# Kernel optimization log

Measured on AMD Instinct MI355X. Metric: run time of the kernel, lower is better.

## Reference

```python
import jax, jax.numpy as jnp
import numpy as np

HIDDEN = 4096
N_HEADS = 32
HEAD_DIM = HIDDEN // N_HEADS
MAX_POS = 2048
ROPE_BASE = 10000.0


def _rope_tables(head_dim, max_pos):
    inv_freq = 1.0 / (ROPE_BASE ** (np.arange(0, head_dim, 2, dtype=np.float32) / head_dim))
    t = np.arange(max_pos, dtype=np.float32)
    freqs = np.einsum('i,j->ij', t, inv_freq)          # [max_pos, head_dim//2]
    emb = np.concatenate([freqs, freqs], axis=-1)       # [max_pos, head_dim]
    return jnp.asarray(np.cos(emb)), jnp.asarray(np.sin(emb))


def _rotate_half(x):
    x1, x2 = jnp.split(x, 2, axis=-1)
    return jnp.concatenate([-x2, x1], axis=-1)


def setup_inputs() -> dict:
    key = jax.random.key(0)
    ks = jax.random.split(key, 5)
    B, S = 1, 2048
    hidden_states = jax.random.normal(ks[0], (B, S, HIDDEN), dtype=jnp.float32)
    # additive causal mask (0 on/below diagonal, large negative above)
    causal = jnp.triu(jnp.full((S, S), -1e9, dtype=jnp.float32), k=1)
    attention_mask = causal[None, None, :, :]
    scale = 0.02
    wq = jax.random.normal(ks[1], (HIDDEN, HIDDEN), dtype=jnp.float32) * scale
    wk = jax.random.normal(ks[2], (HIDDEN, HIDDEN), dtype=jnp.float32) * scale
    wv = jax.random.normal(ks[3], (HIDDEN, HIDDEN), dtype=jnp.float32) * scale
    wo = jax.random.normal(ks[4], (HIDDEN, HIDDEN), dtype=jnp.float32) * scale
    position_ids = jnp.arange(S, dtype=jnp.int64 if jax.config.jax_enable_x64 else jnp.int32)[None, :]
    return {"hidden_states": hidden_states, "attention_mask": attention_mask,
            "wq": wq, "wk": wk, "wv": wv, "wo": wo, "position_ids": position_ids}


def reference(hidden_states, attention_mask, wq, wk, wv, wo, position_ids):
    B, S, H = hidden_states.shape
    cos_tab, sin_tab = _rope_tables(HEAD_DIM, MAX_POS)

    def shape_heads(x):  # [B,S,H] -> [B,nH,S,hd]
        return x.reshape(B, S, N_HEADS, HEAD_DIM).transpose(0, 2, 1, 3)

    # QKV projections (torch Linear: x @ W.T, no bias)
    q = shape_heads(hidden_states @ wq.T)
    k = shape_heads(hidden_states @ wk.T)
    v = shape_heads(hidden_states @ wv.T)

    # RoPE
    cos = cos_tab[position_ids][:, None, :, :]  # [B,1,S,hd]
    sin = sin_tab[position_ids][:, None, :, :]
    q = q * cos + _rotate_half(q) * sin
    k = k * cos + _rotate_half(k) * sin

    # scaled dot-product attention
    scale = 1.0 / jnp.sqrt(jnp.float32(HEAD_DIM))
    scores = jnp.einsum('bhqd,bhkd->bhqk', q, k) * scale
    scores = scores + attention_mask  # broadcast over heads
    scores = jnp.maximum(scores, jnp.finfo(scores.dtype).min)
    probs = jax.nn.softmax(scores, axis=-1)
    attn = jnp.einsum('bhqk,bhkd->bhqd', probs, v)

    # merge heads, output projection
    attn = attn.transpose(0, 2, 1, 3).reshape(B, S, H)
    return attn @ wo.T
```

## Files before the change

kernel.cpp:

```cpp
#include <hip/hip_runtime.h>

typedef __bf16 bf16x8 __attribute__((ext_vector_type(8)));
typedef float f32x4 __attribute__((ext_vector_type(4)));

__device__ __forceinline__ ushort f2bf(float f) {
  uint u = __builtin_bit_cast(uint, f);
  u = (u + 0x7fffu + ((u >> 16) & 1u)) >> 16;
  return (ushort)u;
}
__device__ __forceinline__ float bf2f(ushort h) {
  uint u = ((uint)h) << 16;
  return __builtin_bit_cast(float, u);
}

__device__ __forceinline__ void gload16(const ushort* g, ushort* l) {
  __builtin_amdgcn_global_load_lds(
      (const __attribute__((address_space(1))) unsigned int*)(const void*)g,
      (__attribute__((address_space(3))) unsigned int*)(void*)l, 16, 0, 0);
}

__global__ void cvt_f32_bf16_k(const float* __restrict__ in, ushort* __restrict__ out, int n4) {
  int i = blockIdx.x * blockDim.x + threadIdx.x;
  if (i >= n4) return;
  float4 v = reinterpret_cast<const float4*>(in)[i];
  ushort4 o;
  o.x = f2bf(v.x); o.y = f2bf(v.y); o.z = f2bf(v.z); o.w = f2bf(v.w);
  reinterpret_cast<ushort4*>(out)[i] = o;
}

__global__ void rope_tables_k(float* __restrict__ cosT, float* __restrict__ sinT) {
  int i = blockIdx.x * 256 + threadIdx.x;
  int p = i >> 6, j = i & 63;
  float inv = powf(10000.0f, -(float)j / 64.0f);
  float ang = (float)p * inv;
  cosT[i] = cosf(ang);
  sinT[i] = sinf(ang);
}

__global__ void rope_k(ushort* __restrict__ Q, ushort* __restrict__ K,
                       const float* __restrict__ cosT, const float* __restrict__ sinT,
                       const int* __restrict__ pos) {
  int idx = blockIdx.x * 256 + threadIdx.x;
  int s = idx >> 11;
  int rest = idx & 2047;
  int h = rest >> 6, d = rest & 63;
  int p = pos[s];
  float c = cosT[p * 64 + d], sn = sinT[p * 64 + d];
  size_t base = (size_t)s * 4096 + h * 128 + d;
  float q1 = bf2f(Q[base]), q2 = bf2f(Q[base + 64]);
  Q[base]      = f2bf(q1 * c - q2 * sn);
  Q[base + 64] = f2bf(q2 * c + q1 * sn);
  float k1 = bf2f(K[base]), k2 = bf2f(K[base + 64]);
  K[base]      = f2bf(k1 * c - k2 * sn);
  K[base + 64] = f2bf(k2 * c + k1 * sn);
}

template<typename TA, typename TW, int OMODE>
__global__ __launch_bounds__(256) void gemm_bt(const TA* __restrict__ A, const TW* __restrict__ W,
                                               void* __restrict__ Cout) {
  constexpr int K = 4096, N = 4096;
  constexpr bool BF = (sizeof(TA) == 2);
  __shared__ ushort As[128 * 64];
  __shared__ ushort Ws[128 * 64];
  const int tid = threadIdx.x;
  const int w = tid >> 6, lane = tid & 63, g = lane >> 4, r = lane & 15;
  const int wr = w >> 1, wc = w & 1;
  const int id = blockIdx.x;
  const int xcd = id & 7, slot = id >> 3;
  const int nb = (xcd & 3) * 8 + (slot & 7);
  const int mb = (xcd >> 2) * 8 + (slot >> 3);
  const int m0 = mb * 128, n0 = nb * 128;

  f32x4 acc[4][4];
#pragma unroll
  for (int i = 0; i < 4; i++)
#pragma unroll
    for (int j = 0; j < 4; j++) acc[i][j] = f32x4{0.f, 0.f, 0.f, 0.f};

  for (int k0 = 0; k0 < K; k0 += 64) {
    if (k0) __syncthreads();
    if constexpr (BF) {
#pragma unroll
      for (int i = 0; i < 4; i++) {
        int r0 = (w * 4 + i) * 8;
        int row = r0 + (lane >> 3), c = lane & 7;
        int cs = (c ^ (row & 7)) * 8;
        gload16((const ushort*)A + (size_t)(m0 + row) * K + k0 + cs, &As[r0 * 64]);
        gload16((const ushort*)W + (size_t)(n0 + row) * K + k0 + cs, &Ws[r0 * 64]);
      }
    } else {
#pragma unroll
      for (int i = 0; i < 4; i++) {
        int li = tid + i * 256, row = li >> 3, c = li & 7;
        int cs = (c ^ (row & 7)) * 8;
        float4 v0 = *reinterpret_cast<const float4*>(A + (size_t)(m0 + row) * K + k0 + cs);
        float4 v1 = *reinterpret_cast<const float4*>(A + (size_t)(m0 + row) * K + k0 + cs + 4);
        ushort o[8] = {f2bf(v0.x), f2bf(v0.y), f2bf(v0.z), f2bf(v0.w),
                       f2bf(v1.x), f2bf(v1.y), f2bf(v1.z), f2bf(v1.w)};
        *reinterpret_cast<uint4*>(&As[row * 64 + c * 8]) = *reinterpret_cast<uint4*>(o);
      }
#pragma unroll
      for (int i = 0; i < 4; i++) {
        int li = tid + i * 256, row = li >> 3, c = li & 7;
        int cs = (c ^ (row & 7)) * 8;
        float4 v0 = *reinterpret_cast<const float4*>(W + (size_t)(n0 + row) * K + k0 + cs);
        float4 v1 = *reinterpret_cast<const float4*>(W + (size_t)(n0 + row) * K + k0 + cs + 4);
        ushort o[8] = {f2bf(v0.x), f2bf(v0.y), f2bf(v0.z), f2bf(v0.w),
                       f2bf(v1.x), f2bf(v1.y), f2bf(v1.z), f2bf(v1.w)};
        *reinterpret_cast<uint4*>(&Ws[row * 64 + c * 8]) = *reinterpret_cast<uint4*>(o);
      }
    }
    __syncthreads();

#pragma unroll
    for (int kk = 0; kk < 2; kk++) {
      bf16x8 af[4], bfr[4];
#pragma unroll
      for (int mi = 0; mi < 4; mi++) {
        int row = wr * 64 + mi * 16 + r;
        af[mi] = *reinterpret_cast<const bf16x8*>((const char*)As + row * 128 + (((g + kk * 4) ^ (r & 7)) * 16));
      }
#pragma unroll
      for (int nj = 0; nj < 4; nj++) {
        int row = wc * 64 + nj * 16 + r;
        bfr[nj] = *reinterpret_cast<const bf16x8*>((const char*)Ws + row * 128 + (((g + kk * 4) ^ (r & 7)) * 16));
      }
#pragma unroll
      for (int mi = 0; mi < 4; mi++)
#pragma unroll
        for (int nj = 0; nj < 4; nj++)
          acc[mi][nj] = __builtin_amdgcn_mfma_f32_16x16x32_bf16(af[mi], bfr[nj], acc[mi][nj], 0, 0, 0);
    }
  }

  if constexpr (OMODE == 0) {
    float* C = (float*)Cout;
#pragma unroll
    for (int mi = 0; mi < 4; mi++)
#pragma unroll
      for (int nj = 0; nj < 4; nj++)
#pragma unroll
        for (int j = 0; j < 4; j++) {
          int row = m0 + wr * 64 + mi * 16 + g * 4 + j;
          int col = n0 + wc * 64 + nj * 16 + r;
          C[(size_t)row * N + col] = acc[mi][nj][j];
        }
  } else if constexpr (OMODE == 1) {
    ushort* C = (ushort*)Cout;
#pragma unroll
    for (int mi = 0; mi < 4; mi++)
#pragma unroll
      for (int nj = 0; nj < 4; nj++)
#pragma unroll
        for (int j = 0; j < 4; j++) {
          int row = m0 + wr * 64 + mi * 16 + g * 4 + j;
          int col = n0 + wc * 64 + nj * 16 + r;
          C[(size_t)row * N + col] = f2bf(acc[mi][nj][j]);
        }
  } else {
    ushort* C = (ushort*)Cout;
#pragma unroll
    for (int mi = 0; mi < 4; mi++)
#pragma unroll
      for (int nj = 0; nj < 4; nj++) {
        int col = n0 + wc * 64 + nj * 16 + r;
        int row0 = m0 + wr * 64 + mi * 16 + g * 4;
        ushort4 v;
        v.x = f2bf(acc[mi][nj][0]); v.y = f2bf(acc[mi][nj][1]);
        v.z = f2bf(acc[mi][nj][2]); v.w = f2bf(acc[mi][nj][3]);
        *reinterpret_cast<ushort4*>(C + (size_t)col * 2048 + row0) = v;
      }
  }
}

__global__ __launch_bounds__(256) void attn_fwd(const ushort* __restrict__ Q, const ushort* __restrict__ K,
                                                const ushort* __restrict__ Vt, ushort* __restrict__ O) {
  constexpr int S = 2048, HD = 4096;
  __shared__ ushort Ks[2][64 * 128];
  __shared__ ushort Vs[2][128 * 64];
  __shared__ ushort Ps[4][16 * 64];
  const int id = blockIdx.x;
  const int xcd = id & 7, slot = id >> 3;
  const int h = xcd * 4 + (slot & 3);
  const int qx = slot >> 2;
  const int tid = threadIdx.x;
  const int w = tid >> 6, lane = tid & 63, g = lane >> 4, r = lane & 15;
  const float scale = 0.08838834764831845f;
  const int kRow = lane >> 4, kC = lane & 15;
  const int vRow = lane >> 3, vC = lane & 7;

#pragma unroll 1
  for (int pass = 0; pass < 2; ++pass) {
    const int qtile = pass ? (31 - qx) : qx;
    const int qbase = qtile * 64;
    const int nt = qtile + 1;

    bf16x8 qf[4];
    {
      const int qrow = qbase + w * 16 + r;
#pragma unroll
      for (int dc = 0; dc < 4; dc++)
        qf[dc] = *reinterpret_cast<const bf16x8*>(Q + (size_t)qrow * HD + h * 128 + dc * 32 + g * 8);
    }

    f32x4 o[8];
#pragma unroll
    for (int i = 0; i < 8; i++) o[i] = f32x4{0.f, 0.f, 0.f, 0.f};
    float m[4] = {-3e38f, -3e38f, -3e38f, -3e38f};
    float l[4] = {0.f, 0.f, 0.f, 0.f};

    __syncthreads();
#pragma unroll
    for (int i = 0; i < 4; i++) {
      int kr0 = (w * 4 + i) * 4, krow = kr0 + kRow;
      gload16(K + (size_t)krow * HD + h * 128 + (kC ^ (krow & 7)) * 8, &Ks[0][kr0 * 128]);
      int vr0 = (w * 4 + i) * 8, vrow = vr0 + vRow;
      gload16(Vt + (size_t)(h * 128 + vrow) * S + (vC ^ (vrow & 7)) * 8, &Vs[0][vr0 * 64]);
    }

#pragma unroll 1
    for (int t = 0; t < nt; ++t) {
      const int kv0 = t * 64;
      const int buf = t & 1;
      __syncthreads();
      if (t + 1 < nt) {
        const int kvn = kv0 + 64;
#pragma unroll
        for (int i = 0; i < 4; i++) {
          int kr0 = (w * 4 + i) * 4, krow = kr0 + kRow;
          gload16(K + (size_t)(kvn + krow) * HD + h * 128 + (kC ^ (krow & 7)) * 8, &Ks[buf ^ 1][kr0 * 128]);
          int vr0 = (w * 4 + i) * 8, vrow = vr0 + vRow;
          gload16(Vt + (size_t)(h * 128 + vrow) * S + kvn + (vC ^ (vrow & 7)) * 8, &Vs[buf ^ 1][vr0 * 64]);
        }
      }

      f32x4 sc[4];
      __builtin_amdgcn_s_setprio(1);
#pragma unroll
      for (int c = 0; c < 4; c++) {
        f32x4 tacc = f32x4{0.f, 0.f, 0.f, 0.f};
        const int krow = c * 16 + r;
        const char* kb = (const char*)&Ks[buf][0] + krow * 256;
#pragma unroll
        for (int dc = 0; dc < 4; dc++) {
          bf16x8 kf = *reinterpret_cast<const bf16x8*>(kb + ((dc * 64 + g * 16) ^ ((krow & 7) << 4)));
          tacc = __builtin_amdgcn_mfma_f32_16x16x32_bf16(qf[dc], kf, tacc, 0, 0, 0);
        }
        sc[c] = tacc;
      }
      __builtin_amdgcn_s_setprio(0);

#pragma unroll
      for (int c = 0; c < 4; c++) {
        int kvg = kv0 + c * 16 + r;
#pragma unroll
        for (int j = 0; j < 4; j++) {
          int qg = qbase + w * 16 + g * 4 + j;
          float v = sc[c][j] * scale;
          sc[c][j] = (kvg <= qg) ? v : -1e30f;
        }
      }

      float pm[4], alpha[4], ps[4];
#pragma unroll
      for (int j = 0; j < 4; j++)
        pm[j] = fmaxf(fmaxf(sc[0][j], sc[1][j]), fmaxf(sc[2][j], sc[3][j]));
#pragma unroll
      for (int st = 1; st < 16; st <<= 1) {
        float t0 = __shfl_xor(pm[0], st);
        float t1 = __shfl_xor(pm[1], st);
        float t2 = __shfl_xor(pm[2], st);
        float t3 = __shfl_xor(pm[3], st);
        pm[0] = fmaxf(pm[0], t0); pm[1] = fmaxf(pm[1], t1);
        pm[2] = fmaxf(pm[2], t2); pm[3] = fmaxf(pm[3], t3);
      }
#pragma unroll
      for (int j = 0; j < 4; j++) {
        float mn = fmaxf(m[j], pm[j]);
        alpha[j] = __expf(m[j] - mn);
        m[j] = mn;
        float s0 = __expf(sc[0][j] - mn), s1 = __expf(sc[1][j] - mn);
        float s2 = __expf(sc[2][j] - mn), s3 = __expf(sc[3][j] - mn);
        sc[0][j] = s0; sc[1][j] = s1; sc[2][j] = s2; sc[3][j] = s3;
        ps[j] = (s0 + s1) + (s2 + s3);
      }
#pragma unroll
      for (int st = 1; st < 16; st <<= 1) {
        float t0 = __shfl_xor(ps[0], st);
        float t1 = __shfl_xor(ps[1], st);
        float t2 = __shfl_xor(ps[2], st);
        float t3 = __shfl_xor(ps[3], st);
        ps[0] += t0; ps[1] += t1; ps[2] += t2; ps[3] += t3;
      }
#pragma unroll
      for (int j = 0; j < 4; j++) l[j] = l[j] * alpha[j] + ps[j];

      char* pb = (char*)&Ps[w][0];
#pragma unroll
      for (int j = 0; j < 4; j++) {
        int ql = g * 4 + j;
#pragma unroll
        for (int c = 0; c < 4; c++)
          *reinterpret_cast<ushort*>(pb + (size_t)ql * 128 + ((c * 32 + r * 2) ^ ((ql & 7) << 4))) = f2bf(sc[c][j]);
      }
#pragma unroll
      for (int dc = 0; dc < 8; dc++)
#pragma unroll
        for (int j = 0; j < 4; j++) o[dc][j] *= alpha[j];
      __builtin_amdgcn_s_setprio(1);
#pragma unroll
      for (int c2 = 0; c2 < 2; c2++) {
        bf16x8 pf = *reinterpret_cast<const bf16x8*>(pb + (size_t)r * 128 + ((c2 * 64 + g * 16) ^ ((r & 7) << 4)));
#pragma unroll
        for (int dc = 0; dc < 8; dc++) {
          const int vrow = dc * 16 + r;
          bf16x8 vf = *reinterpret_cast<const bf16x8*>((const char*)&Vs[buf][0] + vrow * 128 + ((c2 * 64 + g * 16) ^ ((vrow & 7) << 4)));
          o[dc] = __builtin_amdgcn_mfma_f32_16x16x32_bf16(pf, vf, o[dc], 0, 0, 0);
        }
      }
      __builtin_amdgcn_s_setprio(0);
    }

#pragma unroll
    for (int dc = 0; dc < 8; dc++)
#pragma unroll
      for (int j = 0; j < 4; j++) {
        float v = o[dc][j] / l[j];
        O[(size_t)(qbase + w * 16 + g * 4 + j) * HD + h * 128 + dc * 16 + r] = f2bf(v);
      }
  }
}

extern "C" void kernel_launch(void* const* d_in, const int* in_sizes, int n_in,
                              void* d_out, int out_size, void* d_ws, size_t ws_size,
                              hipStream_t stream) {
  const float* X  = (const float*)d_in[0];
  const float* Wq = (const float*)d_in[2];
  const float* Wk = (const float*)d_in[3];
  const float* Wv = (const float*)d_in[4];
  const float* Wo = (const float*)d_in[5];
  const int* pos  = (const int*)d_in[6];
  float* out = (float*)d_out;
  char* ws = (char*)d_ws;
  const size_t MB = 1024ull * 1024ull;

  float*  tabC = (float*)(ws + 0);
  float*  tabS = (float*)(ws + 512 * 1024);
  ushort* Qb   = (ushort*)(ws + 1 * MB);
  ushort* Kb   = (ushort*)(ws + 17 * MB);
  ushort* Vt   = (ushort*)(ws + 33 * MB);
  ushort* Ab   = (ushort*)(ws + 49 * MB);
  ushort* Xb   = (ushort*)(ws + 65 * MB);
  ushort* Wb   = (ushort*)(ws + 81 * MB);
  const bool fast = ws_size >= 113 * MB;

  rope_tables_k<<<512, 256, 0, stream>>>(tabC, tabS);

  if (fast) {
    cvt_f32_bf16_k<<<8192, 256, 0, stream>>>(X, Xb, 2097152);
    cvt_f32_bf16_k<<<16384, 256, 0, stream>>>(Wq, Wb, 4194304);
    gemm_bt<ushort, ushort, 1><<<512, 256, 0, stream>>>(Xb, Wb, Qb);
    cvt_f32_bf16_k<<<16384, 256, 0, stream>>>(Wk, Wb, 4194304);
    gemm_bt<ushort, ushort, 1><<<512, 256, 0, stream>>>(Xb, Wb, Kb);
    cvt_f32_bf16_k<<<16384, 256, 0, stream>>>(Wv, Wb, 4194304);
    gemm_bt<ushort, ushort, 2><<<512, 256, 0, stream>>>(Xb, Wb, Vt);
    rope_k<<<16384, 256, 0, stream>>>(Qb, Kb, tabC, tabS, pos);
    attn_fwd<<<512, 256, 0, stream>>>(Qb, Kb, Vt, Ab);
    cvt_f32_bf16_k<<<16384, 256, 0, stream>>>(Wo, Wb, 4194304);
    gemm_bt<ushort, ushort, 0><<<512, 256, 0, stream>>>(Ab, Wb, out);
  } else {
    gemm_bt<float, float, 1><<<512, 256, 0, stream>>>(X, Wq, Qb);
    gemm_bt<float, float, 1><<<512, 256, 0, stream>>>(X, Wk, Kb);
    gemm_bt<float, float, 2><<<512, 256, 0, stream>>>(X, Wv, Vt);
    rope_k<<<16384, 256, 0, stream>>>(Qb, Kb, tabC, tabS, pos);
    attn_fwd<<<512, 256, 0, stream>>>(Qb, Kb, Vt, Ab);
    gemm_bt<ushort, float, 0><<<512, 256, 0, stream>>>(Ab, Wo, out);
  }
}
```

Baseline: 477.2 us.

## Lazy softmax rescaling, exp2 with folded scale, mask only on diagonal tile

Reworks the online-softmax inner loop of the attention kernel. The causal mask is now applied only on the last (diagonal) KV tile. The score scale is folded into a base-2 exponent computed with an FMA and the raw exp2 intrinsic. The running max and the rescaling of O and l are updated only when some row's new max exceeds the old one by more than a threshold, which skips the alpha multiply on most tiles. The bf16 rounding of probabilities becomes a cheaper round-half-up. This trades a small numeric-deviation risk from stale maxima and the coarser rounding for fewer VALU ops per tile.

```diff
diff --git a/kernel.cpp b/kernel.cpp
--- a/kernel.cpp
+++ b/kernel.cpp
@@ -8,9 +8,16 @@
   u = (u + 0x7fffu + ((u >> 16) & 1u)) >> 16;
   return (ushort)u;
 }
+__device__ __forceinline__ ushort f2bf_fast(float f) {
+  uint u = __builtin_bit_cast(uint, f);
+  return (ushort)((u + 0x8000u) >> 16);
+}
 __device__ __forceinline__ float bf2f(ushort h) {
   uint u = ((uint)h) << 16;
   return __builtin_bit_cast(float, u);
+}
+__device__ __forceinline__ float ex2(float x) {
+  return __builtin_amdgcn_exp2f(x);
 }
 
 __device__ __forceinline__ void gload16(const ushort* g, ushort* l) {
@@ -176,6 +183,8 @@
 __global__ __launch_bounds__(256) void attn_fwd(const ushort* __restrict__ Q, const ushort* __restrict__ K,
                                                 const ushort* __restrict__ Vt, ushort* __restrict__ O) {
   constexpr int S = 2048, HD = 4096;
+  constexpr float SC2 = 0.12753102f;
+  constexpr float THR = 90.50967f;
   __shared__ ushort Ks[2][64 * 128];
   __shared__ ushort Vs[2][128 * 64];
   __shared__ ushort Ps[4][16 * 64];
@@ -185,7 +194,6 @@
   const int qx = slot >> 2;
   const int tid = threadIdx.x;
   const int w = tid >> 6, lane = tid & 63, g = lane >> 4, r = lane & 15;
-  const float scale = 0.08838834764831845f;
   const int kRow = lane >> 4, kC = lane & 15;
   const int vRow = lane >> 3, vC = lane & 7;
 
@@ -250,18 +258,19 @@
       }
       __builtin_amdgcn_s_setprio(0);
 
-#pragma unroll
-      for (int c = 0; c < 4; c++) {
-        int kvg = kv0 + c * 16 + r;
-#pragma unroll
-        for (int j = 0; j < 4; j++) {
-          int qg = qbase + w * 16 + g * 4 + j;
-          float v = sc[c][j] * scale;
-          sc[c][j] = (kvg <= qg) ? v : -1e30f;
-        }
-      }
-
-      float pm[4], alpha[4], ps[4];
+      if (t == nt - 1) {
+#pragma unroll
+        for (int c = 0; c < 4; c++) {
+          int kvg = kv0 + c * 16 + r;
+#pragma unroll
+          for (int j = 0; j < 4; j++) {
+            int qg = qbase + w * 16 + g * 4 + j;
+            if (kvg > qg) sc[c][j] = -3e38f;
+          }
+        }
+      }
+
+      float pm[4];
 #pragma unroll
       for (int j = 0; j < 4; j++)
         pm[j] = fmaxf(fmaxf(sc[0][j], sc[1][j]), fmaxf(sc[2][j], sc[3][j]));
@@ -274,15 +283,38 @@
         pm[0] = fmaxf(pm[0], t0); pm[1] = fmaxf(pm[1], t1);
         pm[2] = fmaxf(pm[2], t2); pm[3] = fmaxf(pm[3], t3);
       }
+
+      bool ok = (pm[0] - m[0] <= THR) && (pm[1] - m[1] <= THR) &&
+                (pm[2] - m[2] <= THR) && (pm[3] - m[3] <= THR);
+      if (!__all(ok)) {
+#pragma unroll
+        for (int j = 0; j < 4; j++) {
+          float mn = fmaxf(m[j], pm[j]);
+          float alpha = ex2((m[j] - mn) * SC2);
+          m[j] = mn;
+          l[j] *= alpha;
+#pragma unroll
+          for (int dc = 0; dc < 8; dc++) o[dc][j] *= alpha;
+        }
+      }
+
+      float ps[4];
+      char* pb = (char*)&Ps[w][0];
 #pragma unroll
       for (int j = 0; j < 4; j++) {
-        float mn = fmaxf(m[j], pm[j]);
-        alpha[j] = __expf(m[j] - mn);
-        m[j] = mn;
-        float s0 = __expf(sc[0][j] - mn), s1 = __expf(sc[1][j] - mn);
-        float s2 = __expf(sc[2][j] - mn), s3 = __expf(sc[3][j] - mn);
-        sc[0][j] = s0; sc[1][j] = s1; sc[2][j] = s2; sc[3][j] = s3;
-        ps[j] = (s0 + s1) + (s2 + s3);
+        float mb = m[j] * SC2;
+        float p0 = ex2(__builtin_fmaf(sc[0][j], SC2, -mb));
+        float p1 = ex2(__builtin_fmaf(sc[1][j], SC2, -mb));
+        float p2 = ex2(__builtin_fmaf(sc[2][j], SC2, -mb));
+        float p3 = ex2(__builtin_fmaf(sc[3][j], SC2, -mb));
+        ps[j] = (p0 + p1) + (p2 + p3);
+        int ql = g * 4 + j;
+        char* pr = pb + (size_t)ql * 128;
+        uint sw = (ql & 7) << 4;
+        *reinterpret_cast<ushort*>(pr + ((0 * 32 + r * 2) ^ sw)) = f2bf_fast(p0);
+        *reinterpret_cast<ushort*>(pr + ((1 * 32 + r * 2) ^ sw)) = f2bf_fast(p1);
+        *reinterpret_cast<ushort*>(pr + ((2 * 32 + r * 2) ^ sw)) = f2bf_fast(p2);
+        *reinterpret_cast<ushort*>(pr + ((3 * 32 + r * 2) ^ sw)) = f2bf_fast(p3);
       }
 #pragma unroll
       for (int st = 1; st < 16; st <<= 1) {
@@ -293,20 +325,8 @@
         ps[0] += t0; ps[1] += t1; ps[2] += t2; ps[3] += t3;
       }
 #pragma unroll
-      for (int j = 0; j < 4; j++) l[j] = l[j] * alpha[j] + ps[j];
-
-      char* pb = (char*)&Ps[w][0];
-#pragma unroll
-      for (int j = 0; j < 4; j++) {
-        int ql = g * 4 + j;
-#pragma unroll
-        for (int c = 0; c < 4; c++)
-          *reinterpret_cast<ushort*>(pb + (size_t)ql * 128 + ((c * 32 + r * 2) ^ ((ql & 7) << 4))) = f2bf(sc[c][j]);
-      }
-#pragma unroll
-      for (int dc = 0; dc < 8; dc++)
-#pragma unroll
-        for (int j = 0; j < 4; j++) o[dc][j] *= alpha[j];
+      for (int j = 0; j < 4; j++) l[j] += ps[j];
+
       __builtin_amdgcn_s_setprio(1);
 #pragma unroll
       for (int c2 = 0; c2 < 2; c2++) {
```

New measurement: 470.9 us. Within noise of the previous version (-1.3%).
